# Performance work log

Hardware: AMD Instinct MI355X
Metric: run time of the kernel (lower is better)

## Reference

```python
import jax, jax.numpy as jnp
import numpy as np

N, D, T = 8192, 512, 200000


def _pairwise_sq_dists(x):
    # dist[i,j] = ||x_i - x_j||^2, clamped at 0 like the torch version
    sq = jnp.sum(x * x, axis=1)
    d = sq[:, None] + sq[None, :] - 2.0 * (x @ x.T)
    return jnp.maximum(d, 0.0)


def setup_inputs() -> dict:
    key = jax.random.key(0)
    kx, ky, kt = jax.random.split(key, 3)
    x = jax.random.normal(kx, (N, D), dtype=jnp.float32)
    y = jax.random.normal(ky, (N, D), dtype=jnp.float32)
    norm_s = jnp.ones((1,), dtype=jnp.float32)  # NormalizationLayer learned scale
    triplets = jax.random.randint(kt, (T, 3), 0, N, dtype=jnp.int32)
    return {"x": x, "y": y, "norm_s": norm_s, "triplets": triplets}


def reference(x, y, norm_s, triplets):
    # NormalizationLayer on y (pre_layer is None so x passes through)
    y_n = norm_s * y / jnp.linalg.norm(y, axis=1, keepdims=True)

    d_img = _pairwise_sq_dists(x)
    d_txt = _pairwise_sq_dists(y_n)

    i, j, k = triplets[:, 0], triplets[:, 1], triplets[:, 2]
    # log(1 + exp(d_ij - d_ik)) == softplus
    loss_img = jnp.mean(jax.nn.softplus(d_img[i, j] - d_img[i, k]))
    loss_txt = jnp.mean(jax.nn.softplus(d_txt[i, j] - d_txt[i, k]))
    return (loss_img + loss_txt)[None]  # shape (1,), matching torch output
```

## Files before the change

### kernel.cpp

```cpp
#include <hip/hip_runtime.h>
#include <math.h>

#define NROWS 8192
#define DDIM  512
#define NTRIP 200000
#define BINCAP 64
#define ROWU 128
#define CHUNK2 32
#define TCHUNKS (2 * 2 * NROWS)
#define TBLOCKS (TCHUNKS / 4)

typedef __attribute__((ext_vector_type(2))) float f32x2;

__device__ __forceinline__ float wave_sum_all(float v) {
    #pragma unroll
    for (int off = 32; off > 0; off >>= 1) v += __shfl_xor(v, off, 64);
    return v;
}

template<bool HI>
__device__ __forceinline__ f32x2 cvt2(unsigned int u) {
    return __builtin_amdgcn_cvt_pk_f32_fp8((int)u, HI);
}
__device__ __forceinline__ unsigned int pack4(float a, float b, float c, float d) {
    int v = __builtin_amdgcn_cvt_pk_fp8_f32(a, b, 0, false);
    v = __builtin_amdgcn_cvt_pk_fp8_f32(c, d, v, true);
    return (unsigned int)v;
}

__device__ __forceinline__ float softplus_fast(float z) {
    return fmaxf(z, 0.0f) + __logf(1.0f + __expf(-fabsf(z)));
}

__device__ __forceinline__ float dot32(const uint4 ra, const uint4 rb,
                                       const f32x2* __restrict__ ci) {
    f32x2 a2;
    a2  = cvt2<false>(ra.x) * ci[0];
    a2  = cvt2<true >(ra.x) * ci[1]  + a2;
    a2  = cvt2<false>(ra.y) * ci[2]  + a2;
    a2  = cvt2<true >(ra.y) * ci[3]  + a2;
    a2  = cvt2<false>(ra.z) * ci[4]  + a2;
    a2  = cvt2<true >(ra.z) * ci[5]  + a2;
    a2  = cvt2<false>(ra.w) * ci[6]  + a2;
    a2  = cvt2<true >(ra.w) * ci[7]  + a2;
    a2  = cvt2<false>(rb.x) * ci[8]  + a2;
    a2  = cvt2<true >(rb.x) * ci[9]  + a2;
    a2  = cvt2<false>(rb.y) * ci[10] + a2;
    a2  = cvt2<true >(rb.y) * ci[11] + a2;
    a2  = cvt2<false>(rb.z) * ci[12] + a2;
    a2  = cvt2<true >(rb.z) * ci[13] + a2;
    a2  = cvt2<false>(rb.w) * ci[14] + a2;
    a2  = cvt2<true >(rb.w) * ci[15] + a2;
    return a2.x + a2.y;
}

__global__ __launch_bounds__(256) void prep_kernel(
    const float* __restrict__ x, const float* __restrict__ y,
    const float* __restrict__ norm_s,
    const int* __restrict__ trip, int* __restrict__ count,
    int2* __restrict__ slots,
    unsigned int* __restrict__ xq, unsigned int* __restrict__ yq,
    float2* __restrict__ sq)
{
    const int tid = blockIdx.x * 256 + threadIdx.x;
    if (tid < NTRIP) {
        const int i = trip[3*tid], j = trip[3*tid+1], k = trip[3*tid+2];
        const int c = atomicAdd(&count[i], 1);
        if (c < BINCAP) slots[((size_t)i << 6) + c] = (int2){j, k};
    }

    const int row  = blockIdx.x * 4 + (threadIdx.x >> 6);
    const int lane = threadIdx.x & 63;
    const float4* xr = (const float4*)(x + (size_t)row * DDIM);
    const float4* yr = (const float4*)(y + (size_t)row * DDIM);
    const float4 x0 = xr[lane], x1 = xr[lane + 64];
    const float4 y0 = yr[lane], y1 = yr[lane + 64];

    float sy = y0.x*y0.x + y0.y*y0.y + y0.z*y0.z + y0.w*y0.w
             + y1.x*y1.x + y1.y*y1.y + y1.z*y1.z + y1.w*y1.w;
    sy = wave_sum_all(sy);
    const float scale = norm_s[0] * 32.0f / sqrtf(sy);

    const unsigned int ux0 = pack4(x0.x, x0.y, x0.z, x0.w);
    const unsigned int ux1 = pack4(x1.x, x1.y, x1.z, x1.w);
    const unsigned int uy0 = pack4(y0.x*scale, y0.y*scale, y0.z*scale, y0.w*scale);
    const unsigned int uy1 = pack4(y1.x*scale, y1.y*scale, y1.z*scale, y1.w*scale);

    f32x2 sx2 = {0.f, 0.f}, sy2 = {0.f, 0.f};
    {
        f32x2 a;
        a = cvt2<false>(ux0); sx2 = a*a + sx2;
        a = cvt2<true >(ux0); sx2 = a*a + sx2;
        a = cvt2<false>(ux1); sx2 = a*a + sx2;
        a = cvt2<true >(ux1); sx2 = a*a + sx2;
        a = cvt2<false>(uy0); sy2 = a*a + sy2;
        a = cvt2<true >(uy0); sy2 = a*a + sy2;
        a = cvt2<false>(uy1); sy2 = a*a + sy2;
        a = cvt2<true >(uy1); sy2 = a*a + sy2;
    }
    float sx  = wave_sum_all(sx2.x + sx2.y);
    float sqy = wave_sum_all(sy2.x + sy2.y) * (1.0f / 1024.0f);

    ((uint2*)(xq + (size_t)row * ROWU))[lane] = (uint2){ux0, ux1};
    ((uint2*)(yq + (size_t)row * ROWU))[lane] = (uint2){uy0, uy1};
    if (lane == 0) sq[row] = (float2){sx, sqy};
}

__global__ __launch_bounds__(256) void trip_kernel(
    const unsigned int* __restrict__ xq, const unsigned int* __restrict__ yq,
    const float* __restrict__ sqc, const int* __restrict__ count,
    const int2* __restrict__ slots, float* __restrict__ bpart)
{
    const int tid  = threadIdx.x;
    const int lane = tid & 63;
    const int wv   = tid >> 6;
    const int chunk = blockIdx.x * 4 + wv;
    const int isY  = chunk >> 14;
    const int c    = (chunk >> 13) & 1;
    const int bin  = chunk & (NROWS - 1);

    float acc = 0.0f, corr = 0.0f;
    int n = count[bin];
    n = __builtin_amdgcn_readfirstlane(n < BINCAP ? n : BINCAP);
    int m = n - c * CHUNK2;
    if (m > 0) {
        if (m > CHUNK2) m = CHUNK2;

        const int s = lane & 15;
        const unsigned int* base = isY ? yq : xq;
        const float dscale = isY ? (1.0f / 1024.0f) : 1.0f;

        const uint4* irow = ((const uint4*)(base + (size_t)bin * ROWU)) + (s << 1);
        const uint4 qa = irow[0], qb = irow[1];
        f32x2 ci[16];
        ci[0]=cvt2<false>(qa.x);  ci[1]=cvt2<true>(qa.x);
        ci[2]=cvt2<false>(qa.y);  ci[3]=cvt2<true>(qa.y);
        ci[4]=cvt2<false>(qa.z);  ci[5]=cvt2<true>(qa.z);
        ci[6]=cvt2<false>(qa.w);  ci[7]=cvt2<true>(qa.w);
        ci[8]=cvt2<false>(qb.x);  ci[9]=cvt2<true>(qb.x);
        ci[10]=cvt2<false>(qb.y); ci[11]=cvt2<true>(qb.y);
        ci[12]=cvt2<false>(qb.z); ci[13]=cvt2<true>(qb.z);
        ci[14]=cvt2<false>(qb.w); ci[15]=cvt2<true>(qb.w);

        const float sq_self = sqc[2 * bin + isY];
        const int4* bs4 = (const int4*)(slots + ((size_t)bin << 6) + c * CHUNK2);

        const int iters = (m + 3) >> 2;
        const int npad  = (iters << 2) - m;
        const int sub   = (lane >> 5) & 1;

        for (int it = 0; it < iters; ++it) {
            const int tb = it << 2;
            const int4 q0 = bs4[2 * it];
            const int4 q1 = bs4[2 * it + 1];
            int jA = (lane & 32) ? q0.z : q0.x;
            int kA = (lane & 32) ? q0.w : q0.y;
            int rA = (lane & 16) ? kA : jA;
            rA = (tb + sub < m) ? rA : bin;
            int jB = (lane & 32) ? q1.z : q1.x;
            int kB = (lane & 32) ? q1.w : q1.y;
            int rB = (lane & 16) ? kB : jB;
            rB = (tb + 2 + sub < m) ? rB : bin;

            const uint4* pA = ((const uint4*)(base + (size_t)rA * ROWU)) + (s << 1);
            const uint4* pB = ((const uint4*)(base + (size_t)rB * ROWU)) + (s << 1);
            const uint4 a0 = pA[0], a1 = pA[1];
            const uint4 b0 = pB[0], b1 = pB[1];
            const float svA = sqc[2 * rA + isY];
            const float svB = sqc[2 * rB + isY];

            float pa = dot32(a0, a1, ci);
            float pb = dot32(b0, b1, ci);
            #pragma unroll
            for (int off = 1; off < 16; off <<= 1) {
                pa += __shfl_xor(pa, off, 64);
                pb += __shfl_xor(pb, off, 64);
            }
            const float dA = fmaxf(sq_self + svA - 2.0f * pa * dscale, 0.0f);
            const float dB = fmaxf(sq_self + svB - 2.0f * pb * dscale, 0.0f);
            const float zA = dA - __shfl_xor(dA, 16, 64);
            const float zB = dB - __shfl_xor(dB, 16, 64);
            const float sp = softplus_fast(zA) + softplus_fast(zB);
            acc += (lane & 16) ? 0.0f : sp;
        }
        corr = (float)npad * 16.0f * 0.6931471805599453f;
    }

    acc = wave_sum_all(acc);
    __shared__ float red[4];
    if (lane == 0) red[wv] = acc - corr;
    __syncthreads();
    if (tid == 0) bpart[blockIdx.x] = red[0] + red[1] + red[2] + red[3];
}

__global__ __launch_bounds__(256) void reduce_kernel(
    const float* __restrict__ bpart, float* __restrict__ out)
{
    float s = 0.0f;
    for (int i = threadIdx.x; i < TBLOCKS; i += 256) s += bpart[i];
    s = wave_sum_all(s);
    __shared__ float red[4];
    const int wv = threadIdx.x >> 6, lane = threadIdx.x & 63;
    if (lane == 0) red[wv] = s;
    __syncthreads();
    if (threadIdx.x == 0)
        out[0] = (red[0] + red[1] + red[2] + red[3])
                 * (1.0f / (16.0f * (float)NTRIP));
}

extern "C" void kernel_launch(void* const* d_in, const int* in_sizes, int n_in,
                              void* d_out, int out_size, void* d_ws, size_t ws_size,
                              hipStream_t stream) {
    const float* x      = (const float*)d_in[0];
    const float* y      = (const float*)d_in[1];
    const float* norm_s = (const float*)d_in[2];
    const int*   trip   = (const int*)d_in[3];

    unsigned int* xq    = (unsigned int*)d_ws;
    unsigned int* yq    = xq + (size_t)NROWS * ROWU;
    float2*       sq    = (float2*)(yq + (size_t)NROWS * ROWU);
    int*          count = (int*)(sq + NROWS);
    float*        bpart = (float*)(count + NROWS);
    int2*         slots = (int2*)(bpart + TBLOCKS);

    (void)hipMemsetAsync(count, 0, sizeof(int) * NROWS, stream);
    prep_kernel<<<NROWS / 4, 256, 0, stream>>>(x, y, norm_s, trip, count, slots,
                                               xq, yq, sq);
    trip_kernel<<<TBLOCKS, 256, 0, stream>>>(xq, yq, (const float*)sq, count,
                                             slots, bpart);
    reduce_kernel<<<1, 256, 0, stream>>>(bpart, (float*)d_out);
}
```

Measured before the change: 148.3 us.

## Loop each wave over multiple bins and phases with smaller triplet chunks

Instead of one wave per (modality, chunk, bin) with 32-triplet chunks, each wave now walks 2 phases × 4 chunks of 16 triplets, covering bins staggered across the wave index. The total block count drops (2048 vs 8192) and launch bounds request higher occupancy. The aim is to balance load across waves, since bins have variable counts and many old waves were empty, and to cut per-wave launch and reduction overhead. The cost is serial work per wave and reloading the anchor row for each chunk.

```diff
diff --git a/kernel.cpp b/kernel.cpp
--- a/kernel.cpp
+++ b/kernel.cpp
@@ -6,9 +6,9 @@
 #define NTRIP 200000
 #define BINCAP 64
 #define ROWU 128
-#define CHUNK2 32
-#define TCHUNKS (2 * 2 * NROWS)
-#define TBLOCKS (TCHUNKS / 4)
+#define CHUNK 16
+#define TBLOCKS 2048
+#define NWAVES (TBLOCKS * 4)
 
 typedef __attribute__((ext_vector_type(2))) float f32x2;
 
@@ -106,7 +106,7 @@
     if (lane == 0) sq[row] = (float2){sx, sqy};
 }
 
-__global__ __launch_bounds__(256) void trip_kernel(
+__global__ __launch_bounds__(256, 8) void trip_kernel(
     const unsigned int* __restrict__ xq, const unsigned int* __restrict__ yq,
     const float* __restrict__ sqc, const int* __restrict__ count,
     const int2* __restrict__ slots, float* __restrict__ bpart)
@@ -114,76 +114,80 @@
     const int tid  = threadIdx.x;
     const int lane = tid & 63;
     const int wv   = tid >> 6;
-    const int chunk = blockIdx.x * 4 + wv;
-    const int isY  = chunk >> 14;
-    const int c    = (chunk >> 13) & 1;
-    const int bin  = chunk & (NROWS - 1);
+    const int w    = blockIdx.x * 4 + wv;
+    const int s    = lane & 15;
+    const int sub  = (lane >> 5) & 1;
 
     float acc = 0.0f, corr = 0.0f;
-    int n = count[bin];
-    n = __builtin_amdgcn_readfirstlane(n < BINCAP ? n : BINCAP);
-    int m = n - c * CHUNK2;
-    if (m > 0) {
-        if (m > CHUNK2) m = CHUNK2;
-
-        const int s = lane & 15;
-        const unsigned int* base = isY ? yq : xq;
-        const float dscale = isY ? (1.0f / 1024.0f) : 1.0f;
-
-        const uint4* irow = ((const uint4*)(base + (size_t)bin * ROWU)) + (s << 1);
-        const uint4 qa = irow[0], qb = irow[1];
-        f32x2 ci[16];
-        ci[0]=cvt2<false>(qa.x);  ci[1]=cvt2<true>(qa.x);
-        ci[2]=cvt2<false>(qa.y);  ci[3]=cvt2<true>(qa.y);
-        ci[4]=cvt2<false>(qa.z);  ci[5]=cvt2<true>(qa.z);
-        ci[6]=cvt2<false>(qa.w);  ci[7]=cvt2<true>(qa.w);
-        ci[8]=cvt2<false>(qb.x);  ci[9]=cvt2<true>(qb.x);
-        ci[10]=cvt2<false>(qb.y); ci[11]=cvt2<true>(qb.y);
-        ci[12]=cvt2<false>(qb.z); ci[13]=cvt2<true>(qb.z);
-        ci[14]=cvt2<false>(qb.w); ci[15]=cvt2<true>(qb.w);
-
-        const float sq_self = sqc[2 * bin + isY];
-        const int4* bs4 = (const int4*)(slots + ((size_t)bin << 6) + c * CHUNK2);
-
-        const int iters = (m + 3) >> 2;
-        const int npad  = (iters << 2) - m;
-        const int sub   = (lane >> 5) & 1;
-
-        for (int it = 0; it < iters; ++it) {
-            const int tb = it << 2;
-            const int4 q0 = bs4[2 * it];
-            const int4 q1 = bs4[2 * it + 1];
-            int jA = (lane & 32) ? q0.z : q0.x;
-            int kA = (lane & 32) ? q0.w : q0.y;
-            int rA = (lane & 16) ? kA : jA;
-            rA = (tb + sub < m) ? rA : bin;
-            int jB = (lane & 32) ? q1.z : q1.x;
-            int kB = (lane & 32) ? q1.w : q1.y;
-            int rB = (lane & 16) ? kB : jB;
-            rB = (tb + 2 + sub < m) ? rB : bin;
-
-            const uint4* pA = ((const uint4*)(base + (size_t)rA * ROWU)) + (s << 1);
-            const uint4* pB = ((const uint4*)(base + (size_t)rB * ROWU)) + (s << 1);
-            const uint4 a0 = pA[0], a1 = pA[1];
-            const uint4 b0 = pB[0], b1 = pB[1];
-            const float svA = sqc[2 * rA + isY];
-            const float svB = sqc[2 * rB + isY];
-
-            float pa = dot32(a0, a1, ci);
-            float pb = dot32(b0, b1, ci);
-            #pragma unroll
-            for (int off = 1; off < 16; off <<= 1) {
-                pa += __shfl_xor(pa, off, 64);
-                pb += __shfl_xor(pb, off, 64);
+
+    #pragma unroll 1
+    for (int ph = 0; ph < 2; ++ph) {
+        const unsigned int* base = ph ? yq : xq;
+        const float dscale = ph ? (1.0f / 1024.0f) : 1.0f;
+
+        #pragma unroll 1
+        for (int c = 0; c < 4; ++c) {
+            const int bin = (w + (ph << 10) + (c << 11)) & (NROWS - 1);
+            int n = count[bin];
+            n = __builtin_amdgcn_readfirstlane(n < BINCAP ? n : BINCAP);
+            int m = n - c * CHUNK;
+            if (m <= 0) continue;
+            if (m > CHUNK) m = CHUNK;
+
+            const uint4* irow = ((const uint4*)(base + (size_t)bin * ROWU)) + (s << 1);
+            const uint4 qa = irow[0], qb = irow[1];
+            f32x2 ci[16];
+            ci[0]=cvt2<false>(qa.x);  ci[1]=cvt2<true>(qa.x);
+            ci[2]=cvt2<false>(qa.y);  ci[3]=cvt2<true>(qa.y);
+            ci[4]=cvt2<false>(qa.z);  ci[5]=cvt2<true>(qa.z);
+            ci[6]=cvt2<false>(qa.w);  ci[7]=cvt2<true>(qa.w);
+            ci[8]=cvt2<false>(qb.x);  ci[9]=cvt2<true>(qb.x);
+            ci[10]=cvt2<false>(qb.y); ci[11]=cvt2<true>(qb.y);
+            ci[12]=cvt2<false>(qb.z); ci[13]=cvt2<true>(qb.z);
+            ci[14]=cvt2<false>(qb.w); ci[15]=cvt2<true>(qb.w);
+
+            const float sq_self = sqc[2 * bin + ph];
+            const int4* bs4 = (const int4*)(slots + ((size_t)bin << 6) + c * CHUNK);
+
+            const int iters = (m + 3) >> 2;
+            const int npad  = (iters << 2) - m;
+
+            for (int it = 0; it < iters; ++it) {
+                const int tb = it << 2;
+                const int4 q0 = bs4[2 * it];
+                const int4 q1 = bs4[2 * it + 1];
+                int jA = (lane & 32) ? q0.z : q0.x;
+                int kA = (lane & 32) ? q0.w : q0.y;
+                int rA = (lane & 16) ? kA : jA;
+                rA = (tb + sub < m) ? rA : bin;
+                int jB = (lane & 32) ? q1.z : q1.x;
+                int kB = (lane & 32) ? q1.w : q1.y;
+                int rB = (lane & 16) ? kB : jB;
+                rB = (tb + 2 + sub < m) ? rB : bin;
+
+                const uint4* pA = ((const uint4*)(base + (size_t)rA * ROWU)) + (s << 1);
+                const uint4* pB = ((const uint4*)(base + (size_t)rB * ROWU)) + (s << 1);
+                const uint4 a0 = pA[0], a1 = pA[1];
+                const uint4 b0 = pB[0], b1 = pB[1];
+                const float svA = sqc[2 * rA + ph];
+                const float svB = sqc[2 * rB + ph];
+
+                float pa = dot32(a0, a1, ci);
+                float pb = dot32(b0, b1, ci);
+                #pragma unroll
+                for (int off = 1; off < 16; off <<= 1) {
+                    pa += __shfl_xor(pa, off, 64);
+                    pb += __shfl_xor(pb, off, 64);
+                }
+                const float dA = fmaxf(sq_self + svA - 2.0f * pa * dscale, 0.0f);
+                const float dB = fmaxf(sq_self + svB - 2.0f * pb * dscale, 0.0f);
+                const float zA = dA - __shfl_xor(dA, 16, 64);
+                const float zB = dB - __shfl_xor(dB, 16, 64);
+                const float sp = softplus_fast(zA) + softplus_fast(zB);
+                acc += (lane & 16) ? 0.0f : sp;
             }
-            const float dA = fmaxf(sq_self + svA - 2.0f * pa * dscale, 0.0f);
-            const float dB = fmaxf(sq_self + svB - 2.0f * pb * dscale, 0.0f);
-            const float zA = dA - __shfl_xor(dA, 16, 64);
-            const float zB = dB - __shfl_xor(dB, 16, 64);
-            const float sp = softplus_fast(zA) + softplus_fast(zB);
-            acc += (lane & 16) ? 0.0f : sp;
+            corr += (float)npad * 16.0f * 0.6931471805599453f;
         }
-        corr = (float)npad * 16.0f * 0.6931471805599453f;
     }
 
     acc = wave_sum_all(acc);
```

After: 181.5 us. +22.4%, slower.
